# Performance work log

Measured on AMD Instinct MI355X. Metric: run time of the kernel, lower is better.

Reference implementation:

```python
import jax, jax.numpy as jnp
import numpy as np
import math

T, B, D = 256, 32, 512
H, HD, ETA, R = 8, 64, 4, 4
FEAT = HD * ETA
EPS = 1e-6


def setup_inputs() -> dict:
    key = jax.random.key(0)
    ks = jax.random.split(key, 14)
    w = lambda k, shape: jax.random.normal(k, shape, dtype=jnp.float32) * 0.03
    return {
        'inputs': jax.random.normal(ks[0], (T, B, D), dtype=jnp.float32) * 0.1,
        'terminations': jax.random.randint(ks[1], (T, B), 0, 2).astype(jnp.int32),
        'tilde_k_prev': jnp.zeros((B, R, H, FEAT), jnp.float32),
        'tilde_v_prev': jnp.zeros((B, R, H, HD), jnp.float32),
        's_prev': jnp.zeros((B, H, FEAT), jnp.float32),
        'tick': jnp.zeros((B,), jnp.float32),
        'Wq': w(ks[2], (H * HD, D)), 'Wk': w(ks[3], (H * HD, D)), 'Wv': w(ks[4], (H * HD, D)),
        'Wb': w(ks[5], (H * HD, D)), 'Wg': w(ks[6], (H * HD, D)),
        'Wp1': w(ks[7], (H * ETA, D)), 'Wp2': w(ks[8], (H * ETA, D)), 'Wp3': w(ks[9], (H * ETA, D)),
        'Wo': w(ks[10], (D, H * HD)), 'bo': jnp.zeros((D,), jnp.float32),
    }


def _feature_map(x, p):
    # x: (T,B,H,HD), p: (T,B,H,ETA) -> relu outer product -> (T,B,H,ETA*HD)
    f = jax.nn.relu(x[..., None, :] * p[..., :, None])
    return f.reshape(*f.shape[:3], FEAT)


def _gamma_map(g, p):
    # g in (0,1): (T,B,H,HD); p3 gated by sigmoid so result stays in (0,1)
    f = g[..., None, :] * jax.nn.sigmoid(p)[..., :, None]
    return f.reshape(*f.shape[:3], FEAT)


def _discounted_sum(prev, x, d):
    # s_t = d_t * s_{t-1} + x_t ; returns all T states
    def step(carry, xd):
        xi, di = xd
        carry = di * carry + xi
        return carry, carry
    _, ys = jax.lax.scan(step, prev, (x, d))
    return ys


def reference(inputs, terminations, tilde_k_prev, tilde_v_prev, s_prev, tick,
              Wq, Wk, Wv, Wb, Wg, Wp1, Wp2, Wp3, Wo, bo):
    proj = lambda W, n: jnp.einsum('tbd,ed->tbe', inputs, W).reshape(T, B, H, n)
    q = proj(Wq, HD); k = proj(Wk, HD); v = proj(Wv, HD)
    beta = jax.nn.sigmoid(proj(Wb, HD))
    gamma = jax.nn.sigmoid(proj(Wg, HD))
    p1 = proj(Wp1, ETA); p2 = proj(Wp2, ETA); p3 = proj(Wp3, ETA)

    phi_q = _feature_map(q, p2)      # (T,B,H,FEAT)
    psi_k = _feature_map(k, p1)
    gamma_feat = _gamma_map(gamma, p3)

    omegas = jnp.linspace(-math.pi, math.pi, R).astype(jnp.float32)
    steps = jnp.arange(1, T + 1, dtype=jnp.float32)
    cos_step = jnp.cos(steps[:, None] * omegas)   # (T,R)
    sin_step = jnp.sin(steps[:, None] * omegas)
    ang_tick = tick[:, None] * omegas             # (B,R)
    cos_terms = (jnp.cos(ang_tick)[None] * cos_step[:, None]
                 - jnp.sin(ang_tick)[None] * sin_step[:, None])  # (T,B,R)

    gated_v = v * beta                      # (T,B,H,HD)
    gated_k = psi_k * gamma_feat            # (T,B,H,FEAT)
    ce = cos_terms[..., None, None]         # (T,B,R,1,1)
    values_osc = gated_v[:, :, None] * ce   # (T,B,R,H,HD)
    keys_osc = gated_k[:, :, None] * ce     # (T,B,R,H,FEAT)

    term_mask = (1.0 - terminations.astype(jnp.float32))[..., None, None]  # (T,B,1,1)
    disc_gamma = (1.0 - gamma_feat) * term_mask   # (T,B,H,FEAT)
    disc_beta = (1.0 - beta) * term_mask          # (T,B,H,HD)

    final_keys = _discounted_sum(tilde_k_prev, keys_osc, disc_gamma[:, :, None])
    final_values = _discounted_sum(tilde_v_prev, values_osc, disc_beta[:, :, None])
    final_s = _discounted_sum(s_prev, gated_k, disc_gamma)

    kdq = jnp.einsum('tbrhD,tbhD->tbrh', final_keys, phi_q)
    kv = jnp.einsum('tbrhd,tbrh->tbhd', final_values, kdq)
    norm = jnp.einsum('tbhD,tbhD->tbh', final_s, phi_q)
    attn = kv / (2.0 * R * norm[..., None] + EPS)
    out = jnp.einsum('tbe,de->tbd', attn.reshape(T, B, H * HD), Wo) + bo
    return out
```

## Files before the change

kernel.cpp:

```cpp
#include <hip/hip_runtime.h>
#include <hip/hip_bf16.h>

#define T_N 256
#define B_N 32
#define D_N 512
#define H_N 8
#define HD_N 64
#define ETA_N 4
#define R_N 4
#define FEAT_N 256
#define NCOL 2688
#define TB_N (T_N * B_N)
#define NCHUNK 16
#define CLEN 16

using bf16 = __hip_bfloat16;
typedef __attribute__((ext_vector_type(8))) short short8;
typedef __attribute__((ext_vector_type(4))) float f32x4;
typedef __attribute__((ext_vector_type(4))) unsigned short u16x4;

__device__ __forceinline__ float sigmoidf_(float x) { return 1.f / (1.f + __expf(-x)); }
__device__ __forceinline__ float b2f(unsigned short u) {
  union { unsigned int i; float f; } x; x.i = ((unsigned int)u) << 16; return x.f;
}

__global__ void cast_f32_to_bf16_vec4(const float* __restrict__ src,
                                      bf16* __restrict__ dst, int n4) {
  int i = blockIdx.x * blockDim.x + threadIdx.x;
  if (i < n4) {
    float4 v = reinterpret_cast<const float4*>(src)[i];
    bf16* d = dst + (size_t)i * 4;
    d[0] = __float2bfloat16(v.x);
    d[1] = __float2bfloat16(v.y);
    d[2] = __float2bfloat16(v.z);
    d[3] = __float2bfloat16(v.w);
  }
}

__global__ void build_wcat(const float* __restrict__ Wq, const float* __restrict__ Wk,
                           const float* __restrict__ Wv, const float* __restrict__ Wb,
                           const float* __restrict__ Wg, const float* __restrict__ Wp1,
                           const float* __restrict__ Wp2, const float* __restrict__ Wp3,
                           bf16* __restrict__ Wcat) {
  int i = blockIdx.x * blockDim.x + threadIdx.x;
  if (i >= NCOL * D_N) return;
  int r = i >> 9, k = i & 511;
  float v = 0.f;
  if      (r <  512) v = Wq [(r       ) * D_N + k];
  else if (r < 1024) v = Wk [(r -  512) * D_N + k];
  else if (r < 1536) v = Wv [(r - 1024) * D_N + k];
  else if (r < 2048) v = Wb [(r - 1536) * D_N + k];
  else if (r < 2560) v = Wg [(r - 2048) * D_N + k];
  else if (r < 2592) v = Wp1[(r - 2560) * D_N + k];
  else if (r < 2624) v = Wp2[(r - 2592) * D_N + k];
  else if (r < 2656) v = Wp3[(r - 2624) * D_N + k];
  Wcat[i] = __float2bfloat16(v);
}

template <typename OutT>
__global__ __launch_bounds__(256) void gemm_bt_bf16(
    const bf16* __restrict__ A, const bf16* __restrict__ Bm,
    OutT* __restrict__ C, const float* __restrict__ bias,
    int K, int ldc) {
  __shared__ __align__(16) bf16 As[128 * 32];
  __shared__ __align__(16) bf16 Bs[128 * 32];
  const int tid = threadIdx.x;
  const int w = tid >> 6, l = tid & 63;
  const size_t tm = (size_t)blockIdx.x * 128;
  const size_t tn = (size_t)blockIdx.y * 128;
  const int lr = l & 15, lk8 = (l >> 4) * 8;
  const int wr = (w >> 1) * 64, wc = (w & 1) * 64;
  f32x4 acc[4][4] = {};

  for (int kt = 0; kt < K; kt += 32) {
    __syncthreads();
#pragma unroll
    for (int j = 0; j < 2; ++j) {
      int q = (w * 2 + j) * 64 + l;
      int row = q >> 2, cc = (q & 3) * 8;
      __builtin_amdgcn_global_load_lds(
          (const __attribute__((address_space(1))) void*)(A + (tm + row) * K + kt + cc),
          (__attribute__((address_space(3))) void*)(As + q * 8), 16, 0, 0);
      __builtin_amdgcn_global_load_lds(
          (const __attribute__((address_space(1))) void*)(Bm + (tn + row) * K + kt + cc),
          (__attribute__((address_space(3))) void*)(Bs + q * 8), 16, 0, 0);
    }
    __syncthreads();
    short8 af[4], bfr[4];
#pragma unroll
    for (int i = 0; i < 4; ++i)
      af[i] = *reinterpret_cast<const short8*>(As + (wr + i * 16 + lr) * 32 + lk8);
#pragma unroll
    for (int i = 0; i < 4; ++i)
      bfr[i] = *reinterpret_cast<const short8*>(Bs + (wc + i * 16 + lr) * 32 + lk8);
#pragma unroll
    for (int i = 0; i < 4; ++i)
#pragma unroll
      for (int j = 0; j < 4; ++j)
        acc[i][j] = __builtin_amdgcn_mfma_f32_16x16x32_bf16(af[i], bfr[j], acc[i][j], 0, 0, 0);
  }

  const int oc = l & 15, orow = (l >> 4) * 4;
#pragma unroll
  for (int i = 0; i < 4; ++i)
#pragma unroll
    for (int j = 0; j < 4; ++j) {
      size_t col = tn + wc + j * 16 + oc;
      float bv = bias ? bias[col] : 0.f;
#pragma unroll
      for (int v = 0; v < 4; ++v) {
        size_t row = tm + wr + i * 16 + orow + v;
        float val = acc[i][j][v] + bv;
        if constexpr (__is_same(OutT, bf16))
          C[row * ldc + col] = __float2bfloat16(val);
        else
          C[row * ldc + col] = val;
      }
    }
}

__global__ __launch_bounds__(64) void scan_pass1(
    const unsigned short* __restrict__ proj, const int* __restrict__ term,
    const float* __restrict__ tick, float* __restrict__ PE) {
  const int bc = blockIdx.x;
  const int bh = bc >> 4, c = bc & (NCHUNK - 1);
  const int b = bh >> 3, h = bh & 7;
  const int lane = threadIdx.x;
  const int t0 = c * CLEN;

  float s_st[ETA_N] = {};
  float k_st[ETA_N][R_N] = {};
  float v_st[R_N] = {};
  float Pg[ETA_N] = {1.f, 1.f, 1.f, 1.f};
  float Pb = 1.f;

  float ce[R_N], se[R_N], cw[R_N], sw[R_N];
  const float tk = tick[b];
#pragma unroll
  for (int r = 0; r < R_N; ++r) {
    float w = -3.14159265358979323846f + 2.09439510239319549231f * (float)r;
    float a0 = (tk + (float)(t0 + 1)) * w;
    ce[r] = cosf(a0); se[r] = sinf(a0);
    cw[r] = cosf(w);  sw[r] = sinf(w);
  }

  const int koff = 512 + h * HD_N + lane;
  const unsigned short* rw0 = proj + (size_t)(t0 * B_N + b) * NCOL;
  float nk = b2f(rw0[koff]), nv = b2f(rw0[512 + koff]);
  float nbl = b2f(rw0[1024 + koff]), ngl = b2f(rw0[1536 + koff]);
  u16x4 np1 = *(const u16x4*)(rw0 + 2560 + h * 4);
  u16x4 np3 = *(const u16x4*)(rw0 + 2624 + h * 4);
  int nterm = term[t0 * B_N + b];

  for (int tt = 0; tt < CLEN; ++tt) {
    float k = nk, v = nv, bl = nbl, gl = ngl;
    u16x4 p1 = np1, p3 = np3;
    int tmv = nterm;
    if (tt + 1 < CLEN) {
      const unsigned short* rw = proj + (size_t)((t0 + tt + 1) * B_N + b) * NCOL;
      nk = b2f(rw[koff]); nv = b2f(rw[512 + koff]);
      nbl = b2f(rw[1024 + koff]); ngl = b2f(rw[1536 + koff]);
      np1 = *(const u16x4*)(rw + 2560 + h * 4);
      np3 = *(const u16x4*)(rw + 2624 + h * 4);
      nterm = term[(t0 + tt + 1) * B_N + b];
    }

    float mask  = 1.f - (float)tmv;
    float gamma = sigmoidf_(gl);
    float beta  = sigmoidf_(bl);
    float p1a[4]  = {b2f(p1[0]), b2f(p1[1]), b2f(p1[2]), b2f(p1[3])};
    float sp3a[4] = {sigmoidf_(b2f(p3[0])), sigmoidf_(b2f(p3[1])),
                     sigmoidf_(b2f(p3[2])), sigmoidf_(b2f(p3[3]))};

#pragma unroll
    for (int e = 0; e < ETA_N; ++e) {
      float psi = fmaxf(k * p1a[e], 0.f);
      float gf  = gamma * sp3a[e];
      float gk  = psi * gf;
      float dg  = (1.f - gf) * mask;
      s_st[e] = dg * s_st[e] + gk;
      Pg[e] *= dg;
#pragma unroll
      for (int r = 0; r < R_N; ++r)
        k_st[e][r] = dg * k_st[e][r] + gk * ce[r];
    }
    float gv = v * beta;
    float db = (1.f - beta) * mask;
    Pb *= db;
#pragma unroll
    for (int r = 0; r < R_N; ++r)
      v_st[r] = db * v_st[r] + gv * ce[r];

#pragma unroll
    for (int r = 0; r < R_N; ++r) {
      float c2 = ce[r] * cw[r] - se[r] * sw[r];
      float s2 = se[r] * cw[r] + ce[r] * sw[r];
      ce[r] = c2; se[r] = s2;
    }
  }

  float* pe = PE + (size_t)(c * 256 + bh) * 1856;
#pragma unroll
  for (int e = 0; e < ETA_N; ++e) pe[e * 64 + lane] = Pg[e];
  pe[256 + lane] = Pb;
#pragma unroll
  for (int e = 0; e < ETA_N; ++e) pe[320 + e * 64 + lane] = s_st[e];
#pragma unroll
  for (int e = 0; e < ETA_N; ++e)
#pragma unroll
    for (int r = 0; r < R_N; ++r)
      pe[576 + (e * 4 + r) * 64 + lane] = k_st[e][r];
#pragma unroll
  for (int r = 0; r < R_N; ++r) pe[1600 + r * 64 + lane] = v_st[r];
}

__global__ __launch_bounds__(256) void scan_pass2(
    const float* __restrict__ PE, const float* __restrict__ tkp,
    const float* __restrict__ tvp, const float* __restrict__ sp,
    float* __restrict__ carry) {
  const int elem = blockIdx.x * 256 + threadIdx.x;
  const int bh = blockIdx.y;
  const int b = bh >> 3, h = bh & 7;
  int poff, eoff; float cr;
  if (elem < 256) {
    cr = sp[(b * H_N + h) * FEAT_N + elem];
    poff = elem; eoff = 320 + elem;
  } else if (elem < 1280) {
    int el = elem - 256;
    int e = el >> 8, r = (el >> 6) & 3, d = el & 63;
    cr = tkp[((b * R_N + r) * H_N + h) * FEAT_N + e * 64 + d];
    poff = e * 64 + d; eoff = 576 + el;
  } else {
    int el = elem - 1280;
    int r = el >> 6, d = el & 63;
    cr = tvp[((b * R_N + r) * H_N + h) * HD_N + d];
    poff = 256 + d; eoff = 1600 + el;
  }
  for (int c = 0; c < NCHUNK; ++c) {
    carry[(size_t)(c * 256 + bh) * 1536 + elem] = cr;
    const float* pe = PE + (size_t)(c * 256 + bh) * 1856;
    cr = pe[poff] * cr + pe[eoff];
  }
}

__global__ __launch_bounds__(64) void scan_pass3(
    const unsigned short* __restrict__ proj, const int* __restrict__ term,
    const float* __restrict__ carry, const float* __restrict__ tick,
    bf16* __restrict__ attn) {
  const int bc = blockIdx.x;
  const int bh = bc >> 4, c = bc & (NCHUNK - 1);
  const int b = bh >> 3, h = bh & 7;
  const int lane = threadIdx.x;
  const int t0 = c * CLEN;

  const float* cb = carry + (size_t)(c * 256 + bh) * 1536;
  float s_st[ETA_N], k_st[ETA_N][R_N], v_st[R_N];
#pragma unroll
  for (int e = 0; e < ETA_N; ++e) s_st[e] = cb[e * 64 + lane];
#pragma unroll
  for (int e = 0; e < ETA_N; ++e)
#pragma unroll
    for (int r = 0; r < R_N; ++r)
      k_st[e][r] = cb[256 + (e * 4 + r) * 64 + lane];
#pragma unroll
  for (int r = 0; r < R_N; ++r) v_st[r] = cb[1280 + r * 64 + lane];

  float ce[R_N], se[R_N], cw[R_N], sw[R_N];
  const float tk = tick[b];
#pragma unroll
  for (int r = 0; r < R_N; ++r) {
    float w = -3.14159265358979323846f + 2.09439510239319549231f * (float)r;
    float a0 = (tk + (float)(t0 + 1)) * w;
    ce[r] = cosf(a0); se[r] = sinf(a0);
    cw[r] = cosf(w);  sw[r] = sinf(w);
  }

  const int qoff = h * HD_N + lane;
  const unsigned short* rw0 = proj + (size_t)(t0 * B_N + b) * NCOL;
  float nq = b2f(rw0[qoff]), nk = b2f(rw0[512 + qoff]), nv = b2f(rw0[1024 + qoff]);
  float nbl = b2f(rw0[1536 + qoff]), ngl = b2f(rw0[2048 + qoff]);
  u16x4 np1 = *(const u16x4*)(rw0 + 2560 + h * 4);
  u16x4 np2 = *(const u16x4*)(rw0 + 2592 + h * 4);
  u16x4 np3 = *(const u16x4*)(rw0 + 2624 + h * 4);
  int nterm = term[t0 * B_N + b];

  for (int tt = 0; tt < CLEN; ++tt) {
    float q = nq, k = nk, v = nv, bl = nbl, gl = ngl;
    u16x4 p1 = np1, p2 = np2, p3 = np3;
    int tmv = nterm;
    if (tt + 1 < CLEN) {
      const unsigned short* rw = proj + (size_t)((t0 + tt + 1) * B_N + b) * NCOL;
      nq = b2f(rw[qoff]); nk = b2f(rw[512 + qoff]); nv = b2f(rw[1024 + qoff]);
      nbl = b2f(rw[1536 + qoff]); ngl = b2f(rw[2048 + qoff]);
      np1 = *(const u16x4*)(rw + 2560 + h * 4);
      np2 = *(const u16x4*)(rw + 2592 + h * 4);
      np3 = *(const u16x4*)(rw + 2624 + h * 4);
      nterm = term[(t0 + tt + 1) * B_N + b];
    }

    float mask  = 1.f - (float)tmv;
    float gamma = sigmoidf_(gl);
    float beta  = sigmoidf_(bl);
    float p1a[4]  = {b2f(p1[0]), b2f(p1[1]), b2f(p1[2]), b2f(p1[3])};
    float p2a[4]  = {b2f(p2[0]), b2f(p2[1]), b2f(p2[2]), b2f(p2[3])};
    float sp3a[4] = {sigmoidf_(b2f(p3[0])), sigmoidf_(b2f(p3[1])),
                     sigmoidf_(b2f(p3[2])), sigmoidf_(b2f(p3[3]))};

    float norm_p = 0.f, kdq0 = 0.f, kdq1 = 0.f, kdq2 = 0.f, kdq3 = 0.f;
#pragma unroll
    for (int e = 0; e < ETA_N; ++e) {
      float psi = fmaxf(k * p1a[e], 0.f);
      float gf  = gamma * sp3a[e];
      float gk  = psi * gf;
      float dg  = (1.f - gf) * mask;
      float phi = fmaxf(q * p2a[e], 0.f);
      s_st[e] = dg * s_st[e] + gk;
      norm_p += s_st[e] * phi;
      k_st[e][0] = dg * k_st[e][0] + gk * ce[0]; kdq0 += k_st[e][0] * phi;
      k_st[e][1] = dg * k_st[e][1] + gk * ce[1]; kdq1 += k_st[e][1] * phi;
      k_st[e][2] = dg * k_st[e][2] + gk * ce[2]; kdq2 += k_st[e][2] * phi;
      k_st[e][3] = dg * k_st[e][3] + gk * ce[3]; kdq3 += k_st[e][3] * phi;
    }
#pragma unroll
    for (int m = 1; m < 64; m <<= 1) {
      norm_p += __shfl_xor(norm_p, m);
      kdq0 += __shfl_xor(kdq0, m);
      kdq1 += __shfl_xor(kdq1, m);
      kdq2 += __shfl_xor(kdq2, m);
      kdq3 += __shfl_xor(kdq3, m);
    }
    float gv = v * beta;
    float db = (1.f - beta) * mask;
    v_st[0] = db * v_st[0] + gv * ce[0];
    v_st[1] = db * v_st[1] + gv * ce[1];
    v_st[2] = db * v_st[2] + gv * ce[2];
    v_st[3] = db * v_st[3] + gv * ce[3];
    float kv = v_st[0] * kdq0 + v_st[1] * kdq1 + v_st[2] * kdq2 + v_st[3] * kdq3;
    float a = kv / (8.f * norm_p + 1e-6f);
    attn[((size_t)((t0 + tt) * B_N + b) * H_N + h) * HD_N + lane] = __float2bfloat16(a);
#pragma unroll
    for (int r = 0; r < R_N; ++r) {
      float c2 = ce[r] * cw[r] - se[r] * sw[r];
      float s2 = se[r] * cw[r] + ce[r] * sw[r];
      ce[r] = c2; se[r] = s2;
    }
  }
}

extern "C" void kernel_launch(void* const* d_in, const int* in_sizes, int n_in,
                              void* d_out, int out_size, void* d_ws, size_t ws_size,
                              hipStream_t stream) {
  const float* x    = (const float*)d_in[0];
  const int*   term = (const int*)  d_in[1];
  const float* tkp  = (const float*)d_in[2];
  const float* tvp  = (const float*)d_in[3];
  const float* sp   = (const float*)d_in[4];
  const float* tick = (const float*)d_in[5];
  const float* Wq   = (const float*)d_in[6];
  const float* Wk   = (const float*)d_in[7];
  const float* Wv   = (const float*)d_in[8];
  const float* Wb   = (const float*)d_in[9];
  const float* Wg   = (const float*)d_in[10];
  const float* Wp1  = (const float*)d_in[11];
  const float* Wp2  = (const float*)d_in[12];
  const float* Wp3  = (const float*)d_in[13];
  const float* Wo   = (const float*)d_in[14];
  const float* bo   = (const float*)d_in[15];
  float* out = (float*)d_out;

  char* ws = (char*)d_ws;
  bf16*  projb = (bf16*)(ws);
  bf16*  attn  = (bf16*)(ws + 44040192);
  bf16*  Xb    = (bf16*)(ws + 52428800);
  bf16*  Wcat  = (bf16*)(ws + 60817408);
  float* PE    = (float*)(ws + 52428800);
  float* carry = (float*)(ws + 82837504);
  bf16*  Wob   = (bf16*)(ws + 52428800);

  cast_f32_to_bf16_vec4<<<4096, 256, 0, stream>>>(x, Xb, TB_N * D_N / 4);
  build_wcat<<<(NCOL * D_N + 255) / 256, 256, 0, stream>>>(Wq, Wk, Wv, Wb, Wg, Wp1, Wp2, Wp3, Wcat);

  gemm_bt_bf16<bf16><<<dim3(TB_N / 128, NCOL / 128), 256, 0, stream>>>(
      Xb, Wcat, projb, nullptr, D_N, NCOL);

  const unsigned short* proju = (const unsigned short*)projb;
  scan_pass1<<<B_N * H_N * NCHUNK, 64, 0, stream>>>(proju, term, tick, PE);
  scan_pass2<<<dim3(6, 256), 256, 0, stream>>>(PE, tkp, tvp, sp, carry);
  cast_f32_to_bf16_vec4<<<256, 256, 0, stream>>>(Wo, Wob, D_N * D_N / 4);
  scan_pass3<<<B_N * H_N * NCHUNK, 64, 0, stream>>>(proju, term, carry, tick, attn);

  gemm_bt_bf16<float><<<dim3(TB_N / 128, D_N / 128), 256, 0, stream>>>(
      attn, Wob, out, bo, D_N, D_N);
}
```

Before: 239.1 us.

## Double scan chunk count and write carries in place over chunk end states

```diff
diff --git a/kernel.cpp b/kernel.cpp
--- a/kernel.cpp
+++ b/kernel.cpp
@@ -11,8 +11,8 @@
 #define FEAT_N 256
 #define NCOL 2688
 #define TB_N (T_N * B_N)
-#define NCHUNK 16
-#define CLEN 16
+#define NCHUNK 32
+#define CLEN 8
 
 using bf16 = __hip_bfloat16;
 typedef __attribute__((ext_vector_type(8))) short short8;
@@ -119,11 +119,11 @@
     }
 }
 
-__global__ __launch_bounds__(64) void scan_pass1(
+__global__ __launch_bounds__(64, 8) void scan_pass1(
     const unsigned short* __restrict__ proj, const int* __restrict__ term,
-    const float* __restrict__ tick, float* __restrict__ PE) {
+    const float* __restrict__ tick, float* __restrict__ Pa, float* __restrict__ Ea) {
   const int bc = blockIdx.x;
-  const int bh = bc >> 4, c = bc & (NCHUNK - 1);
+  const int bh = bc >> 5, c = bc & (NCHUNK - 1);
   const int b = bh >> 3, h = bh & 7;
   const int lane = threadIdx.x;
   const int t0 = c * CLEN;
@@ -199,61 +199,68 @@
     }
   }
 
-  float* pe = PE + (size_t)(c * 256 + bh) * 1856;
-#pragma unroll
-  for (int e = 0; e < ETA_N; ++e) pe[e * 64 + lane] = Pg[e];
-  pe[256 + lane] = Pb;
-#pragma unroll
-  for (int e = 0; e < ETA_N; ++e) pe[320 + e * 64 + lane] = s_st[e];
+  float* pa = Pa + (size_t)(c * 256 + bh) * 320;
+#pragma unroll
+  for (int e = 0; e < ETA_N; ++e) pa[e * 64 + lane] = Pg[e];
+  pa[256 + lane] = Pb;
+  float* ea = Ea + (size_t)(c * 256 + bh) * 1536;
+#pragma unroll
+  for (int e = 0; e < ETA_N; ++e) ea[e * 64 + lane] = s_st[e];
 #pragma unroll
   for (int e = 0; e < ETA_N; ++e)
 #pragma unroll
     for (int r = 0; r < R_N; ++r)
-      pe[576 + (e * 4 + r) * 64 + lane] = k_st[e][r];
-#pragma unroll
-  for (int r = 0; r < R_N; ++r) pe[1600 + r * 64 + lane] = v_st[r];
+      ea[256 + (e * 4 + r) * 64 + lane] = k_st[e][r];
+#pragma unroll
+  for (int r = 0; r < R_N; ++r) ea[1280 + r * 64 + lane] = v_st[r];
 }
 
 __global__ __launch_bounds__(256) void scan_pass2(
-    const float* __restrict__ PE, const float* __restrict__ tkp,
-    const float* __restrict__ tvp, const float* __restrict__ sp,
-    float* __restrict__ carry) {
+    const float* __restrict__ Pa, float* __restrict__ Ea,
+    const float* __restrict__ tkp, const float* __restrict__ tvp,
+    const float* __restrict__ sp) {
   const int elem = blockIdx.x * 256 + threadIdx.x;
   const int bh = blockIdx.y;
   const int b = bh >> 3, h = bh & 7;
   int poff, eoff; float cr;
   if (elem < 256) {
     cr = sp[(b * H_N + h) * FEAT_N + elem];
-    poff = elem; eoff = 320 + elem;
+    poff = elem; eoff = elem;
   } else if (elem < 1280) {
     int el = elem - 256;
     int e = el >> 8, r = (el >> 6) & 3, d = el & 63;
     cr = tkp[((b * R_N + r) * H_N + h) * FEAT_N + e * 64 + d];
-    poff = e * 64 + d; eoff = 576 + el;
+    poff = e * 64 + d; eoff = elem;
   } else {
     int el = elem - 1280;
     int r = el >> 6, d = el & 63;
     cr = tvp[((b * R_N + r) * H_N + h) * HD_N + d];
-    poff = 256 + d; eoff = 1600 + el;
-  }
+    poff = 256 + d; eoff = elem;
+  }
+  const size_t sP = 256 * 320, sE = 256 * 1536;
+  size_t ip = (size_t)bh * 320 + poff;
+  size_t ie = (size_t)bh * 1536 + eoff;
+  float p = Pa[ip], e = Ea[ie];
   for (int c = 0; c < NCHUNK; ++c) {
-    carry[(size_t)(c * 256 + bh) * 1536 + elem] = cr;
-    const float* pe = PE + (size_t)(c * 256 + bh) * 1856;
-    cr = pe[poff] * cr + pe[eoff];
-  }
-}
-
-__global__ __launch_bounds__(64) void scan_pass3(
+    float pn = 0.f, en = 0.f;
+    if (c + 1 < NCHUNK) { pn = Pa[ip + sP]; en = Ea[ie + sE]; }
+    Ea[ie] = cr;
+    cr = p * cr + e;
+    p = pn; e = en; ip += sP; ie += sE;
+  }
+}
+
+__global__ __launch_bounds__(64, 8) void scan_pass3(
     const unsigned short* __restrict__ proj, const int* __restrict__ term,
-    const float* __restrict__ carry, const float* __restrict__ tick,
+    const float* __restrict__ Ea, const float* __restrict__ tick,
     bf16* __restrict__ attn) {
   const int bc = blockIdx.x;
-  const int bh = bc >> 4, c = bc & (NCHUNK - 1);
+  const int bh = bc >> 5, c = bc & (NCHUNK - 1);
   const int b = bh >> 3, h = bh & 7;
   const int lane = threadIdx.x;
   const int t0 = c * CLEN;
 
-  const float* cb = carry + (size_t)(c * 256 + bh) * 1536;
+  const float* cb = Ea + (size_t)(c * 256 + bh) * 1536;
   float s_st[ETA_N], k_st[ETA_N][R_N], v_st[R_N];
 #pragma unroll
   for (int e = 0; e < ETA_N; ++e) s_st[e] = cb[e * 64 + lane];
@@ -370,12 +377,12 @@
 
   char* ws = (char*)d_ws;
   bf16*  projb = (bf16*)(ws);
-  bf16*  attn  = (bf16*)(ws + 44040192);
-  bf16*  Xb    = (bf16*)(ws + 52428800);
-  bf16*  Wcat  = (bf16*)(ws + 60817408);
-  float* PE    = (float*)(ws + 52428800);
-  float* carry = (float*)(ws + 82837504);
-  bf16*  Wob   = (bf16*)(ws + 52428800);
+  float* Ea    = (float*)(ws + 44040192);
+  float* Pa    = (float*)(ws + 94371840);
+  bf16*  Xb    = (bf16*)(ws + 44040192);
+  bf16*  Wcat  = (bf16*)(ws + 52428800);
+  bf16*  attn  = (bf16*)(ws + 94371840);
+  bf16*  Wob   = (bf16*)(ws + 94371840 + 8388608);
 
   cast_f32_to_bf16_vec4<<<4096, 256, 0, stream>>>(x, Xb, TB_N * D_N / 4);
   build_wcat<<<(NCOL * D_N + 255) / 256, 256, 0, stream>>>(Wq, Wk, Wv, Wb, Wg, Wp1, Wp2, Wp3, Wcat);
@@ -384,10 +391,10 @@
       Xb, Wcat, projb, nullptr, D_N, NCOL);
 
   const unsigned short* proju = (const unsigned short*)projb;
-  scan_pass1<<<B_N * H_N * NCHUNK, 64, 0, stream>>>(proju, term, tick, PE);
-  scan_pass2<<<dim3(6, 256), 256, 0, stream>>>(PE, tkp, tvp, sp, carry);
+  scan_pass1<<<B_N * H_N * NCHUNK, 64, 0, stream>>>(proju, term, tick, Pa, Ea);
+  scan_pass2<<<dim3(6, 256), 256, 0, stream>>>(Pa, Ea, tkp, tvp, sp);
   cast_f32_to_bf16_vec4<<<256, 256, 0, stream>>>(Wo, Wob, D_N * D_N / 4);
-  scan_pass3<<<B_N * H_N * NCHUNK, 64, 0, stream>>>(proju, term, carry, tick, attn);
+  scan_pass3<<<B_N * H_N * NCHUNK, 64, 0, stream>>>(proju, term, Ea, tick, attn);
 
   gemm_bt_bf16<float><<<dim3(TB_N / 128, D_N / 128), 256, 0, stream>>>(
       attn, Wob, out, bo, D_N, D_N);
```

Measured after the change: 327.7 us. +37.1%, slower.
